# Performance work log

Measured on AMD Instinct MI355X. Metric: run time of the kernel, lower is better.

The kernel has to match this reference:

```python
import jax, jax.numpy as jnp
import numpy as np

B, T, M, P = 256, 256, 256, 256  # batch, timesteps, encoder hidden m, decoder hidden p


def setup_inputs() -> dict:
    key = jax.random.key(0)
    ks = jax.random.split(key, 12)
    def n(k, shape, s=0.05):
        return jax.random.normal(k, shape, dtype=jnp.float32) * s
    return {
        "data": n(ks[0], (B, T - 1, 1), 1.0),          # decoder inputs y_1..y_{T-1}
        "encoder_h": n(ks[1], (B, T, M), 1.0),          # encoder hidden states
        "h0": jnp.zeros((B, P), jnp.float32),
        "s0": jnp.zeros((B, P), jnp.float32),
        # dense: Dense(1) on concat([x, context]) -> input dim 1+M
        "Wd": n(ks[2], (1 + M, 1)), "bd": jnp.zeros((1,), jnp.float32),
        # decoder LSTM (Keras gate order i,f,c,o): kernel (1,4P), recurrent (P,4P)
        "Wk": n(ks[3], (1, 4 * P)), "Wr": n(ks[4], (P, 4 * P)), "bl": jnp.zeros((4 * P,), jnp.float32),
        # temporal attention: W: 2P->M, U: M->M, v: M->1
        "Ww": n(ks[5], (2 * P, M)), "bw": jnp.zeros((M,), jnp.float32),
        "Wu": n(ks[6], (M, M)), "bu": jnp.zeros((M,), jnp.float32),
        "Wv": n(ks[7], (M, 1)), "bv": jnp.zeros((1,), jnp.float32),
        # output head: densevb: P+M -> 1, denseWb: 1 -> P
        "Wvb": n(ks[8], (P + M, 1)), "bvb": jnp.zeros((1,), jnp.float32),
        "Wwb": n(ks[9], (1, P)), "bwb": jnp.zeros((P,), jnp.float32),
    }


def reference(data, encoder_h, h0, s0, Wd, bd, Wk, Wr, bl, Ww, bw,
              Wu, bu, Wv, bv, Wvb, bvb, Wwb, bwb):
    # Hoist U(encoder_h) out of the time loop: it does not depend on t (same math).
    Ue = encoder_h @ Wu + bu                      # (B, T, M)
    xs = jnp.transpose(data, (1, 0, 2))           # (T-1, B, 1) for scan
    ctx0 = jnp.zeros((data.shape[0], Ue.shape[-1]), data.dtype)  # initial context (B, M)

    def step(carry, x_t):
        h, s, ctx = carry                          # (B,P), (B,P), (B,M)
        # y_tilde = Dense(1)(concat([x_t, context]))
        y = jnp.concatenate([x_t, ctx], axis=-1) @ Wd + bd        # (B, 1)
        # single-step Keras LSTM cell, gates i, f, c, o
        z = y @ Wk + h @ Wr + bl                   # (B, 4P)
        i, f, g, o = jnp.split(z, 4, axis=-1)
        s_new = jax.nn.sigmoid(f) * s + jax.nn.sigmoid(i) * jnp.tanh(g)
        h_new = jax.nn.sigmoid(o) * jnp.tanh(s_new)
        # temporal attention: l = v(tanh(W(repeat(concat[h,s])) + U(encoder_h)))
        dsc = jnp.concatenate([h_new, s_new], axis=-1) @ Ww + bw  # (B, M)
        l = jnp.tanh(dsc[:, None, :] + Ue) @ Wv + bv              # (B, T, 1)
        beta = jax.nn.softmax(l, axis=1)                          # softmax over time axis
        # context = beta^T @ encoder_h -> (B, M)
        ctx_new = jnp.sum(beta * encoder_h, axis=1)
        return (h_new, s_new, ctx_new), None

    (h, s, ctx), _ = jax.lax.scan(step, (h0, s0, ctx0), xs)
    cat = jnp.concatenate([h, ctx], axis=-1)[:, None, :]          # (B, 1, P+M)
    # denseWb(densevb(concatenated)): (P+M)->1 then 1->P, as in the source
    return (cat @ Wvb + bvb) @ Wwb + bwb                          # (B, 1, P)
```

## Files before the change

### kernel.cpp

```cpp
#include <hip/hip_runtime.h>
#include <hip/hip_bf16.h>

#define B 256
#define T 256
#define M 256
#define P 256
#define TSTEPS 255
#define NT 1024

typedef unsigned int uint;
typedef _Float16 hf2 __attribute__((ext_vector_type(2)));

__device__ __forceinline__ float fast_tanh(float x) {
    float e = exp2f(x * 2.885390082f);
    return 1.f - 2.f * __builtin_amdgcn_rcpf(e + 1.f);
}
__device__ __forceinline__ float fast_sigmoid(float x) {
    float e = exp2f(-x * 1.442695041f);
    return __builtin_amdgcn_rcpf(1.f + e);
}

#if defined(__has_builtin)
#if __has_builtin(__builtin_amdgcn_fdot2)
#define HAVE_FDOT2 1
#endif
#endif

__device__ __forceinline__ float dot2(uint a, uint b, float c) {
#ifdef HAVE_FDOT2
    return __builtin_amdgcn_fdot2(__builtin_bit_cast(hf2, a),
                                  __builtin_bit_cast(hf2, b), c, false);
#else
    hf2 x = __builtin_bit_cast(hf2, a), y = __builtin_bit_cast(hf2, b);
    return c + (float)x.x * (float)y.x + (float)x.y * (float)y.y;
#endif
}

__device__ __forceinline__ uint pk16(float a, float b) {
    return __builtin_bit_cast(uint, __builtin_amdgcn_cvt_pkrtz(a, b));
}

__global__ __launch_bounds__(256) void ue_gemm(
    const float* __restrict__ enc, const float* __restrict__ Wu,
    const float* __restrict__ bu, _Float16* __restrict__ Ue16)
{
    __shared__ float At[32][256];
    const int r0 = blockIdx.x * 32;
    const int tid = threadIdx.x;

    #pragma unroll 4
    for (int i = 0; i < 32; ++i)
        At[i][tid] = enc[(size_t)(r0 + i) * 256 + tid];
    __syncthreads();

    float acc[32];
    #pragma unroll
    for (int r = 0; r < 32; ++r) acc[r] = 0.f;

    for (int k = 0; k < 256; k += 4) {
        float w0 = Wu[(size_t)(k + 0) * 256 + tid];
        float w1 = Wu[(size_t)(k + 1) * 256 + tid];
        float w2 = Wu[(size_t)(k + 2) * 256 + tid];
        float w3 = Wu[(size_t)(k + 3) * 256 + tid];
        #pragma unroll
        for (int r = 0; r < 32; ++r) {
            float4 a4 = *(const float4*)&At[r][k];
            acc[r] += a4.x * w0 + a4.y * w1 + a4.z * w2 + a4.w * w3;
        }
    }
    float bub = bu[tid];
    #pragma unroll 4
    for (int r = 0; r < 32; ++r)
        Ue16[(size_t)(r0 + r) * 256 + tid] =
            (_Float16)exp2f(1.442695041f * (acc[r] + bub));
}

__global__ __launch_bounds__(256) void wr_cvt(
    const float* __restrict__ Wr, uint4* __restrict__ Wsz)
{
    int i = blockIdx.x * 256 + threadIdx.x;
    int kc = i >> 10, c = i & 1023;
    const float* s = Wr + (size_t)kc * 8 * 1024 + c;
    uint4 o;
    o.x = pk16(s[0 * 1024], s[1 * 1024]);
    o.y = pk16(s[2 * 1024], s[3 * 1024]);
    o.z = pk16(s[4 * 1024], s[5 * 1024]);
    o.w = pk16(s[6 * 1024], s[7 * 1024]);
    Wsz[i] = o;
}

__global__ __launch_bounds__(256) void ww_cvt(
    const float* __restrict__ Ww, uint4* __restrict__ Wwsz)
{
    int i = blockIdx.x * 256 + threadIdx.x;
    int kk = i >> 8, m = i & 255;
    const float* s = Ww + (size_t)kk * 8 * 256 + m;
    uint4 o;
    o.x = pk16(s[0 * 256], s[1 * 256]);
    o.y = pk16(s[2 * 256], s[3 * 256]);
    o.z = pk16(s[4 * 256], s[5 * 256]);
    o.w = pk16(s[6 * 256], s[7 * 256]);
    Wwsz[i] = o;
}

__global__ __launch_bounds__(NT, 4) void decoder_scan(
    const float* __restrict__ data,
    const float* __restrict__ h0,  const float* __restrict__ s0,
    const float* __restrict__ Wd,  const float* __restrict__ bd,
    const float* __restrict__ Wk,  const float* __restrict__ bl,
    const float* __restrict__ bw,
    const float* __restrict__ Wv,  const float* __restrict__ bv,
    const float* __restrict__ Wvb, const float* __restrict__ bvb,
    const float* __restrict__ Wwb, const float* __restrict__ bwb,
    const float* __restrict__ enc,
    const _Float16* __restrict__ Ue16g,
    const uint4* __restrict__ Wsz, const uint4* __restrict__ Wwsz,
    float* __restrict__ out)
{
    const int b    = blockIdx.x;
    const int tid  = threadIdx.x;
    const int lane = tid & 63;
    const int wave = tid >> 6;

    __shared__ _Float16 ue_lds[T * M];
    __shared__ float h_lds[P], s_lds[P];
    __shared__ __align__(16) uint hs2[128 + 4 + 128];
    __shared__ float z_lds[4 * 257];
    __shared__ __align__(16) uint  edup[2][132];
    __shared__ __align__(16) float wv2dup[2][264];
    __shared__ float el_lds[T];
    __shared__ float g_lds[T];
    __shared__ float ctx_lds[M];
    __shared__ __align__(16) float sred[8], yred[8];
    __shared__ float ya[4];
    __shared__ float data_lds[TSTEPS + 1];

    uint* h2_lds = hs2;
    uint* s2_lds = hs2 + 132;

    {
        const uint4* src = (const uint4*)(Ue16g + (size_t)b * T * M);
        uint4* dst = (uint4*)ue_lds;
        #pragma unroll
        for (int i = 0; i < 8; ++i) {
            int g = tid + i * NT;
            uint4 v = src[g];
            int r = g >> 5, lin = g & 31;
            int phys = (lin & 16) | ((lin ^ (2 * r + (lin >> 4))) & 15);
            dst[(r << 5) + phys] = v;
        }
    }
    if (tid < 256) {
        float hv = h0[b * 256 + tid], sv = s0[b * 256 + tid];
        h_lds[tid] = hv; s_lds[tid] = sv; ctx_lds[tid] = 0.f;
        float w2 = 2.f * Wv[tid];
        wv2dup[0][tid] = w2; wv2dup[1][tid] = w2;
        float hv1 = __shfl_down(hv, 1, 64);
        float sv1 = __shfl_down(sv, 1, 64);
        if (!(tid & 1)) {
            h2_lds[tid >> 1] = pk16(hv, hv1);
            s2_lds[tid >> 1] = pk16(sv, sv1);
        }
    }
    if (tid < 8) { sred[tid] = 1.f; yred[tid] = 0.f; }
    if (tid < TSTEPS) data_lds[tid] = data[b * TSTEPS + tid];

    const float Wd0 = Wd[0], bd0 = bd[0];
    const int   gate = tid & 3, uu = tid >> 2;
    const int   cp  = gate * 256 + uu;
    const int   cpi = gate * 257 + uu;
    const float wkp = Wk[cp], blp = bl[cp];

    const float* encB = enc + (size_t)b * T * M;

    {
        float w0 = Wd[1 + lane * 4], w1 = Wd[2 + lane * 4];
        float w2 = Wd[3 + lane * 4], w3 = Wd[4 + lane * 4];
        for (int i = 0; i < 16; ++i) {
            int tp = wave * 16 + i;
            float4 e4 = *(const float4*)&encB[(size_t)tp * 256 + lane * 4];
            float p = e4.x * w0 + e4.y * w1 + e4.z * w2 + e4.w * w3;
            #pragma unroll
            for (int mm = 32; mm >= 1; mm >>= 1) p += __shfl_xor(p, mm, 64);
            if (lane == 0) g_lds[tp] = p;
        }
    }
    __syncthreads();

    const uint4* h2u4 = (const uint4*)h2_lds;
    const uint4* s2u4 = (const uint4*)s2_lds;

    {
        const uint4* wc = Wsz + tid;
        float acc = 0.f;
        #pragma unroll 4
        for (int kc = 0; kc < 32; ++kc) {
            uint4 w = wc[kc << 10];
            uint4 h = h2u4[kc];
            acc = dot2(w.x, h.x, acc); acc = dot2(w.y, h.y, acc);
            acc = dot2(w.z, h.z, acc); acc = dot2(w.w, h.w, acc);
        }
        z_lds[(tid >> 8) * 257 + (tid & 255)] = acc;
    }
    __syncthreads();

    const int aw  = wave - 8;
    const int aid = (tid >= 512) ? (tid - 512) : 0;
    const int dm  = aid >> 1;
    const int dkh = aid & 1;
    const int ekey = aid & 15;
    const float bwm = bw[dm];
    const uint4* wwp  = Wwsz + (dkh << 13) + dm;
    const uint4* uecT = (const uint4*)ue_lds + (aid << 4);
    const uint4*  edT = (const uint4*)(&edup[dkh][0]) + (dkh << 4);
    const float4* wvT = (const float4*)(&wv2dup[dkh][0]) + (dkh << 5);
    const uint4* wcA = Wsz + tid;
    const uint4* wcB = Wsz + tid + 512;

    float accA = 0.f, accB = 0.f;

    for (int t = 0; t < TSTEPS; ++t) {
        {
            float4 sa = *(const float4*)&sred[0], sb = *(const float4*)&sred[4];
            float4 yaa = *(const float4*)&yred[0], yab = *(const float4*)&yred[4];
            float S = sa.x + sa.y + sa.z + sa.w + sb.x + sb.y + sb.z + sb.w;
            float Y = yaa.x + yaa.y + yaa.z + yaa.w + yab.x + yab.y + yab.z + yab.w;
            float ys = Y * __builtin_amdgcn_rcpf(S) + data_lds[t] * Wd0 + bd0;
            float zc = z_lds[cpi] + ys * wkp + blp;
            float nl = (gate == 2) ? fast_tanh(zc) : fast_sigmoid(zc);
            float n1 = __shfl_xor(nl, 1, 64);
            float n2 = __shfl_xor(nl, 2, 64);
            float n3 = __shfl_xor(nl, 3, 64);
            float hn = 0.f, snv = 0.f;
            if (gate == 0) {
                float s_old = s_lds[uu];
                snv = n1 * s_old + nl * n2;
                hn  = n3 * fast_tanh(snv);
                s_lds[uu] = snv; h_lds[uu] = hn;
            }
            float hn4 = __shfl_down(hn, 4, 64);
            float sn4 = __shfl_down(snv, 4, 64);
            if ((tid & 7) == 0) {
                h2_lds[uu >> 1] = pk16(hn, hn4);
                s2_lds[uu >> 1] = pk16(snv, sn4);
            }
        }
        __syncthreads();

        if (wave < 8) {
            accA = 0.f; accB = 0.f;
            #pragma unroll 4
            for (int kc = 0; kc < 16; ++kc) {
                uint4 wA = wcA[kc << 10], wB = wcB[kc << 10];
                uint4 h = h2u4[kc];
                accA = dot2(wA.x, h.x, accA); accA = dot2(wA.y, h.y, accA);
                accA = dot2(wA.z, h.z, accA); accA = dot2(wA.w, h.w, accA);
                accB = dot2(wB.x, h.x, accB); accB = dot2(wB.y, h.y, accB);
                accB = dot2(wB.z, h.z, accB); accB = dot2(wB.w, h.w, accB);
            }
        } else {
            const uint4* cat4 = dkh ? s2u4 : h2u4;
            float a = 0.f;
            #pragma unroll 8
            for (int i = 0; i < 32; ++i) {
                uint4 w = wwp[i << 8];
                uint4 c = cat4[i];
                a = dot2(w.x, c.x, a); a = dot2(w.y, c.y, a);
                a = dot2(w.z, c.z, a); a = dot2(w.w, c.w, a);
            }
            a += __shfl_xor(a, 1, 64);
            float ed = exp2f(1.442695041f * (a + bwm));
            float ed2 = __shfl_xor(ed, 2, 64);
            if ((aid & 3) == 0) {
                uint u = pk16(ed, ed2);
                edup[0][dm >> 1] = u;
                edup[1][dm >> 1] = u;
            }
        }
        __syncthreads();

        if (wave < 8) {
            #pragma unroll 4
            for (int kc = 16; kc < 32; ++kc) {
                uint4 wA = wcA[kc << 10], wB = wcB[kc << 10];
                uint4 h = h2u4[kc];
                accA = dot2(wA.x, h.x, accA); accA = dot2(wA.y, h.y, accA);
                accA = dot2(wA.z, h.z, accA); accA = dot2(wA.w, h.w, accA);
                accB = dot2(wB.x, h.x, accB); accB = dot2(wB.y, h.y, accB);
                accB = dot2(wB.z, h.z, accB); accB = dot2(wB.w, h.w, accB);
            }
            z_lds[(tid >> 8) * 257 + (tid & 255)] = accA;
            z_lds[(2 + (tid >> 8)) * 257 + (tid & 255)] = accB;
        } else {
            __builtin_amdgcn_s_setprio(1);
            float pl = 0.f;
            #pragma unroll 4
            for (int jj = 0; jj < 16; ++jj) {
                uint4 u = uecT[jj ^ ekey];
                uint4 d = edT[jj];
                float4 wA = wvT[jj * 2], wB = wvT[jj * 2 + 1];
                hf2 p0 = __builtin_bit_cast(hf2, u.x) * __builtin_bit_cast(hf2, d.x);
                hf2 p1 = __builtin_bit_cast(hf2, u.y) * __builtin_bit_cast(hf2, d.y);
                hf2 p2 = __builtin_bit_cast(hf2, u.z) * __builtin_bit_cast(hf2, d.z);
                hf2 p3 = __builtin_bit_cast(hf2, u.w) * __builtin_bit_cast(hf2, d.w);
                p0 = p0 * p0; p1 = p1 * p1; p2 = p2 * p2; p3 = p3 * p3;
                {
                    float a0 = fminf((float)p0.x, 1e18f) + 1.f;
                    float a1 = fminf((float)p0.y, 1e18f) + 1.f;
                    float qq = __builtin_amdgcn_rcpf(a0 * a1);
                    pl = fmaf(wA.x, a1 * qq, pl);
                    pl = fmaf(wA.y, a0 * qq, pl);
                }
                {
                    float a0 = fminf((float)p1.x, 1e18f) + 1.f;
                    float a1 = fminf((float)p1.y, 1e18f) + 1.f;
                    float qq = __builtin_amdgcn_rcpf(a0 * a1);
                    pl = fmaf(wA.z, a1 * qq, pl);
                    pl = fmaf(wA.w, a0 * qq, pl);
                }
                {
                    float a0 = fminf((float)p2.x, 1e18f) + 1.f;
                    float a1 = fminf((float)p2.y, 1e18f) + 1.f;
                    float qq = __builtin_amdgcn_rcpf(a0 * a1);
                    pl = fmaf(wB.x, a1 * qq, pl);
                    pl = fmaf(wB.y, a0 * qq, pl);
                }
                {
                    float a0 = fminf((float)p3.x, 1e18f) + 1.f;
                    float a1 = fminf((float)p3.y, 1e18f) + 1.f;
                    float qq = __builtin_amdgcn_rcpf(a0 * a1);
                    pl = fmaf(wB.z, a1 * qq, pl);
                    pl = fmaf(wB.w, a0 * qq, pl);
                }
            }
            pl += __shfl_xor(pl, 1, 64);
            float ev = exp2f(-1.442695041f * pl);
            if (!dkh) el_lds[dm] = ev;
            float yg = ev * g_lds[dm];
            #pragma unroll
            for (int mm = 2; mm <= 32; mm <<= 1) {
                ev += __shfl_xor(ev, mm, 64);
                yg += __shfl_xor(yg, mm, 64);
            }
            if (lane == 0) { sred[aw] = ev; yred[aw] = yg; }
            __builtin_amdgcn_s_setprio(0);
        }
        __syncthreads();
    }

    {
        float S;
        {
            float4 sa = *(const float4*)&sred[0], sb = *(const float4*)&sred[4];
            S = sa.x + sa.y + sa.z + sa.w + sb.x + sb.y + sb.z + sb.w;
        }
        float a0 = 0.f, a1 = 0.f, a2 = 0.f, a3 = 0.f;
        for (int i = 0; i < 16; ++i) {
            int tp = wave * 16 + i;
            float w = el_lds[tp];
            float4 e4 = *(const float4*)&encB[(size_t)tp * 256 + lane * 4];
            a0 += w * e4.x; a1 += w * e4.y; a2 += w * e4.z; a3 += w * e4.w;
        }
        atomicAdd(&ctx_lds[lane * 4 + 0], a0);
        atomicAdd(&ctx_lds[lane * 4 + 1], a1);
        atomicAdd(&ctx_lds[lane * 4 + 2], a2);
        atomicAdd(&ctx_lds[lane * 4 + 3], a3);
        __syncthreads();

        float qp = 0.f;
        if (tid < 256) {
            float ctx = ctx_lds[tid] * __builtin_amdgcn_rcpf(S);
            qp = h_lds[tid] * Wvb[tid] + ctx * Wvb[256 + tid];
        }
        if (wave < 4) {
            #pragma unroll
            for (int mm = 32; mm >= 1; mm >>= 1) qp += __shfl_xor(qp, mm, 64);
            if (lane == 0) ya[wave] = qp;
        }
        __syncthreads();
        if (tid < 256) {
            float qv = ya[0] + ya[1] + ya[2] + ya[3] + bvb[0];
            out[b * 256 + tid] = qv * Wwb[tid] + bwb[tid];
        }
    }
}

extern "C" void kernel_launch(void* const* d_in, const int* in_sizes, int n_in,
                              void* d_out, int out_size, void* d_ws, size_t ws_size,
                              hipStream_t stream) {
    const float* data = (const float*)d_in[0];
    const float* enc  = (const float*)d_in[1];
    const float* h0   = (const float*)d_in[2];
    const float* s0   = (const float*)d_in[3];
    const float* Wd   = (const float*)d_in[4];
    const float* bd   = (const float*)d_in[5];
    const float* Wk   = (const float*)d_in[6];
    const float* Wr   = (const float*)d_in[7];
    const float* bl   = (const float*)d_in[8];
    const float* Ww   = (const float*)d_in[9];
    const float* bw   = (const float*)d_in[10];
    const float* Wu   = (const float*)d_in[11];
    const float* bu   = (const float*)d_in[12];
    const float* Wv   = (const float*)d_in[13];
    const float* bv   = (const float*)d_in[14];
    const float* Wvb  = (const float*)d_in[15];
    const float* bvb  = (const float*)d_in[16];
    const float* Wwb  = (const float*)d_in[17];
    const float* bwb  = (const float*)d_in[18];

    _Float16* Ue16 = (_Float16*)d_ws;
    uint4* Wsz  = (uint4*)((char*)d_ws + (32ull << 20));
    uint4* Wwsz = (uint4*)((char*)d_ws + (32ull << 20) + (512ull << 10));
    float* out = (float*)d_out;

    hipLaunchKernelGGL(ue_gemm, dim3((B * T) / 32), dim3(256), 0, stream,
                       enc, Wu, bu, Ue16);
    hipLaunchKernelGGL(wr_cvt, dim3(128), dim3(256), 0, stream, Wr, Wsz);
    hipLaunchKernelGGL(ww_cvt, dim3(64), dim3(256), 0, stream, Ww, Wwsz);
    hipLaunchKernelGGL(decoder_scan, dim3(B), dim3(NT), 0, stream,
                       data, h0, s0, Wd, bd, Wk, bl, bw,
                       Wv, bv, Wvb, bvb, Wwb, bwb,
                       enc, Ue16, Wsz, Wwsz, out);
}
```

Measured before the change: 2.848 ms.

## Split recurrence and attention waves with spin-flag sync and register-cached weights

```diff
diff --git a/kernel.cpp b/kernel.cpp
--- a/kernel.cpp
+++ b/kernel.cpp
@@ -7,6 +7,8 @@
 #define P 256
 #define TSTEPS 255
 #define NT 1024
+#define RG 6
+#define RA 8
 
 typedef unsigned int uint;
 typedef _Float16 hf2 __attribute__((ext_vector_type(2)));
@@ -134,6 +136,7 @@
     __shared__ __align__(16) float sred[8], yred[8];
     __shared__ float ya[4];
     __shared__ float data_lds[TSTEPS + 1];
+    __shared__ int aflag;
 
     uint* h2_lds = hs2;
     uint* s2_lds = hs2 + 132;
@@ -150,6 +153,7 @@
             dst[(r << 5) + phys] = v;
         }
     }
+    if (tid == 0) aflag = 0;
     if (tid < 256) {
         float hv = h0[b * 256 + tid], sv = s0[b * 256 + tid];
         h_lds[tid] = hv; s_lds[tid] = sv; ctx_lds[tid] = 0.f;
@@ -166,11 +170,6 @@
     if (tid < TSTEPS) data_lds[tid] = data[b * TSTEPS + tid];
 
     const float Wd0 = Wd[0], bd0 = bd[0];
-    const int   gate = tid & 3, uu = tid >> 2;
-    const int   cp  = gate * 256 + uu;
-    const int   cpi = gate * 257 + uu;
-    const float wkp = Wk[cp], blp = bl[cp];
-
     const float* encB = enc + (size_t)b * T * M;
 
     {
@@ -204,65 +203,134 @@
     }
     __syncthreads();
 
-    const int aw  = wave - 8;
-    const int aid = (tid >= 512) ? (tid - 512) : 0;
-    const int dm  = aid >> 1;
-    const int dkh = aid & 1;
-    const int ekey = aid & 15;
-    const float bwm = bw[dm];
-    const uint4* wwp  = Wwsz + (dkh << 13) + dm;
-    const uint4* uecT = (const uint4*)ue_lds + (aid << 4);
-    const uint4*  edT = (const uint4*)(&edup[dkh][0]) + (dkh << 4);
-    const float4* wvT = (const float4*)(&wv2dup[dkh][0]) + (dkh << 5);
-    const uint4* wcA = Wsz + tid;
-    const uint4* wcB = Wsz + tid + 512;
-
-    float accA = 0.f, accB = 0.f;
-
-    for (int t = 0; t < TSTEPS; ++t) {
-        {
-            float4 sa = *(const float4*)&sred[0], sb = *(const float4*)&sred[4];
-            float4 yaa = *(const float4*)&yred[0], yab = *(const float4*)&yred[4];
-            float S = sa.x + sa.y + sa.z + sa.w + sb.x + sb.y + sb.z + sb.w;
-            float Y = yaa.x + yaa.y + yaa.z + yaa.w + yab.x + yab.y + yab.z + yab.w;
-            float ys = Y * __builtin_amdgcn_rcpf(S) + data_lds[t] * Wd0 + bd0;
-            float zc = z_lds[cpi] + ys * wkp + blp;
-            float nl = (gate == 2) ? fast_tanh(zc) : fast_sigmoid(zc);
-            float n1 = __shfl_xor(nl, 1, 64);
-            float n2 = __shfl_xor(nl, 2, 64);
-            float n3 = __shfl_xor(nl, 3, 64);
-            float hn = 0.f, snv = 0.f;
-            if (gate == 0) {
-                float s_old = s_lds[uu];
-                snv = n1 * s_old + nl * n2;
-                hn  = n3 * fast_tanh(snv);
-                s_lds[uu] = snv; h_lds[uu] = hn;
-            }
-            float hn4 = __shfl_down(hn, 4, 64);
-            float sn4 = __shfl_down(snv, 4, 64);
-            if ((tid & 7) == 0) {
-                h2_lds[uu >> 1] = pk16(hn, hn4);
-                s2_lds[uu >> 1] = pk16(snv, sn4);
-            }
-        }
-        __syncthreads();
-
-        if (wave < 8) {
-            accA = 0.f; accB = 0.f;
+    if (wave < 8) {
+        const int gate = tid & 3, uu0 = tid >> 2, uu1 = uu0 + 128;
+        const int cz0 = gate * 257 + uu0, cz1 = gate * 257 + uu1;
+        const float wk0 = Wk[gate * 256 + uu0], bl0 = bl[gate * 256 + uu0];
+        const float wk1 = Wk[gate * 256 + uu1], bl1 = bl[gate * 256 + uu1];
+        const int zr = tid >> 8, zc = tid & 255;
+        const uint4* wcA = Wsz + tid;
+        const uint4* wcB = Wsz + tid + 512;
+        uint4 rA[RG], rB[RG];
+        #pragma unroll
+        for (int kc = 0; kc < RG; ++kc) { rA[kc] = wcA[kc << 10]; rB[kc] = wcB[kc << 10]; }
+
+        for (int t = 0; t < TSTEPS; ++t) {
+            uint4 pA0 = wcA[(RG + 0) << 10], pB0 = wcB[(RG + 0) << 10];
+            uint4 pA1 = wcA[(RG + 1) << 10], pB1 = wcB[(RG + 1) << 10];
+
+            {
+                float4 sa = *(const float4*)&sred[0], sb = *(const float4*)&sred[4];
+                float4 yaa = *(const float4*)&yred[0], yab = *(const float4*)&yred[4];
+                float S = sa.x + sa.y + sa.z + sa.w + sb.x + sb.y + sb.z + sb.w;
+                float Y = yaa.x + yaa.y + yaa.z + yaa.w + yab.x + yab.y + yab.z + yab.w;
+                float ys = Y * __builtin_amdgcn_rcpf(S) + data_lds[t] * Wd0 + bd0;
+                float zc0 = z_lds[cz0] + ys * wk0 + bl0;
+                float zc1 = z_lds[cz1] + ys * wk1 + bl1;
+                float nl0 = (gate == 2) ? fast_tanh(zc0) : fast_sigmoid(zc0);
+                float nl1 = (gate == 2) ? fast_tanh(zc1) : fast_sigmoid(zc1);
+                float a1 = __shfl_xor(nl0, 1, 64);
+                float a2 = __shfl_xor(nl0, 2, 64);
+                float a3 = __shfl_xor(nl0, 3, 64);
+                float b1 = __shfl_xor(nl1, 1, 64);
+                float b2 = __shfl_xor(nl1, 2, 64);
+                float b3 = __shfl_xor(nl1, 3, 64);
+                float hn0 = 0.f, sv0 = 0.f, hn1 = 0.f, sv1 = 0.f;
+                if (gate == 0) {
+                    sv0 = a1 * s_lds[uu0] + nl0 * a2;
+                    hn0 = a3 * fast_tanh(sv0);
+                    sv1 = b1 * s_lds[uu1] + nl1 * b2;
+                    hn1 = b3 * fast_tanh(sv1);
+                    s_lds[uu0] = sv0; h_lds[uu0] = hn0;
+                    s_lds[uu1] = sv1; h_lds[uu1] = hn1;
+                }
+                float hd0 = __shfl_down(hn0, 4, 64), sd0 = __shfl_down(sv0, 4, 64);
+                float hd1 = __shfl_down(hn1, 4, 64), sd1 = __shfl_down(sv1, 4, 64);
+                if ((tid & 7) == 0) {
+                    h2_lds[uu0 >> 1] = pk16(hn0, hd0); s2_lds[uu0 >> 1] = pk16(sv0, sd0);
+                    h2_lds[uu1 >> 1] = pk16(hn1, hd1); s2_lds[uu1 >> 1] = pk16(sv1, sd1);
+                }
+            }
+            __syncthreads();
+            float a0 = 0.f, a1 = 0.f;
+            #pragma unroll
+            for (int kc = 0; kc < RG; ++kc) {
+                uint4 h = h2u4[kc];
+                a0 = dot2(rA[kc].x, h.x, a0); a0 = dot2(rA[kc].y, h.y, a0);
+                a0 = dot2(rA[kc].z, h.z, a0); a0 = dot2(rA[kc].w, h.w, a0);
+                a1 = dot2(rB[kc].x, h.x, a1); a1 = dot2(rB[kc].y, h.y, a1);
+                a1 = dot2(rB[kc].z, h.z, a1); a1 = dot2(rB[kc].w, h.w, a1);
+            }
+            {
+                uint4 h = h2u4[RG];
+                a0 = dot2(pA0.x, h.x, a0); a0 = dot2(pA0.y, h.y, a0);
+                a0 = dot2(pA0.z, h.z, a0); a0 = dot2(pA0.w, h.w, a0);
+                a1 = dot2(pB0.x, h.x, a1); a1 = dot2(pB0.y, h.y, a1);
+                a1 = dot2(pB0.z, h.z, a1); a1 = dot2(pB0.w, h.w, a1);
+            }
+            {
+                uint4 h = h2u4[RG + 1];
+                a0 = dot2(pA1.x, h.x, a0); a0 = dot2(pA1.y, h.y, a0);
+                a0 = dot2(pA1.z, h.z, a0); a0 = dot2(pA1.w, h.w, a0);
+                a1 = dot2(pB1.x, h.x, a1); a1 = dot2(pB1.y, h.y, a1);
+                a1 = dot2(pB1.z, h.z, a1); a1 = dot2(pB1.w, h.w, a1);
+            }
             #pragma unroll 4
-            for (int kc = 0; kc < 16; ++kc) {
+            for (int kc = RG + 2; kc < 32; ++kc) {
                 uint4 wA = wcA[kc << 10], wB = wcB[kc << 10];
                 uint4 h = h2u4[kc];
-                accA = dot2(wA.x, h.x, accA); accA = dot2(wA.y, h.y, accA);
-                accA = dot2(wA.z, h.z, accA); accA = dot2(wA.w, h.w, accA);
-                accB = dot2(wB.x, h.x, accB); accB = dot2(wB.y, h.y, accB);
-                accB = dot2(wB.z, h.z, accB); accB = dot2(wB.w, h.w, accB);
-            }
-        } else {
-            const uint4* cat4 = dkh ? s2u4 : h2u4;
+                a0 = dot2(wA.x, h.x, a0); a0 = dot2(wA.y, h.y, a0);
+                a0 = dot2(wA.z, h.z, a0); a0 = dot2(wA.w, h.w, a0);
+                a1 = dot2(wB.x, h.x, a1); a1 = dot2(wB.y, h.y, a1);
+                a1 = dot2(wB.z, h.z, a1); a1 = dot2(wB.w, h.w, a1);
+            }
+            z_lds[zr * 257 + zc] = a0;
+            z_lds[(2 + zr) * 257 + zc] = a1;
+            __syncthreads();
+        }
+    } else {
+        const int aw  = wave - 8;
+        const int aid = tid - 512;
+        const int dm  = aid >> 1;
+        const int dkh = aid & 1;
+        const int ekey = aid & 15;
+        const float bwm = bw[dm];
+        const uint4* wwp  = Wwsz + (dkh << 13) + dm;
+        const uint4* uecT = (const uint4*)ue_lds + (aid << 4);
+        const uint4*  edT = (const uint4*)(&edup[dkh][0]) + (dkh << 4);
+        const float4* wvT = (const float4*)(&wv2dup[dkh][0]) + (dkh << 5);
+        const uint4* cat4 = dkh ? s2u4 : h2u4;
+        uint4 rW[RA];
+        #pragma unroll
+        for (int i = 0; i < RA; ++i) rW[i] = wwp[i << 8];
+
+        for (int t = 0; t < TSTEPS; ++t) {
+            uint4 e0 = wwp[(RA + 0) << 8], e1 = wwp[(RA + 1) << 8];
+            uint4 e2 = wwp[(RA + 2) << 8], e3 = wwp[(RA + 3) << 8];
+            __syncthreads();
             float a = 0.f;
-            #pragma unroll 8
-            for (int i = 0; i < 32; ++i) {
+            #pragma unroll
+            for (int i = 0; i < RA; ++i) {
+                uint4 c = cat4[i];
+                a = dot2(rW[i].x, c.x, a); a = dot2(rW[i].y, c.y, a);
+                a = dot2(rW[i].z, c.z, a); a = dot2(rW[i].w, c.w, a);
+            }
+            {
+                uint4 c = cat4[RA + 0];
+                a = dot2(e0.x, c.x, a); a = dot2(e0.y, c.y, a);
+                a = dot2(e0.z, c.z, a); a = dot2(e0.w, c.w, a);
+                c = cat4[RA + 1];
+                a = dot2(e1.x, c.x, a); a = dot2(e1.y, c.y, a);
+                a = dot2(e1.z, c.z, a); a = dot2(e1.w, c.w, a);
+                c = cat4[RA + 2];
+                a = dot2(e2.x, c.x, a); a = dot2(e2.y, c.y, a);
+                a = dot2(e2.z, c.z, a); a = dot2(e2.w, c.w, a);
+                c = cat4[RA + 3];
+                a = dot2(e3.x, c.x, a); a = dot2(e3.y, c.y, a);
+                a = dot2(e3.z, c.z, a); a = dot2(e3.w, c.w, a);
+            }
+            #pragma unroll 4
+            for (int i = RA + 4; i < 32; ++i) {
                 uint4 w = wwp[i << 8];
                 uint4 c = cat4[i];
                 a = dot2(w.x, c.x, a); a = dot2(w.y, c.y, a);
@@ -276,22 +344,12 @@
                 edup[0][dm >> 1] = u;
                 edup[1][dm >> 1] = u;
             }
-        }
-        __syncthreads();
-
-        if (wave < 8) {
-            #pragma unroll 4
-            for (int kc = 16; kc < 32; ++kc) {
-                uint4 wA = wcA[kc << 10], wB = wcB[kc << 10];
-                uint4 h = h2u4[kc];
-                accA = dot2(wA.x, h.x, accA); accA = dot2(wA.y, h.y, accA);
-                accA = dot2(wA.z, h.z, accA); accA = dot2(wA.w, h.w, accA);
-                accB = dot2(wB.x, h.x, accB); accB = dot2(wB.y, h.y, accB);
-                accB = dot2(wB.z, h.z, accB); accB = dot2(wB.w, h.w, accB);
-            }
-            z_lds[(tid >> 8) * 257 + (tid & 255)] = accA;
-            z_lds[(2 + (tid >> 8)) * 257 + (tid & 255)] = accB;
-        } else {
+            __threadfence_block();
+            if (lane == 0) atomicAdd(&aflag, 1);
+            const int tgt = 8 * (t + 1);
+            while (*(volatile int*)&aflag < tgt) {}
+            __threadfence_block();
+
             __builtin_amdgcn_s_setprio(1);
             float pl = 0.f;
             #pragma unroll 4
@@ -344,8 +402,8 @@
             }
             if (lane == 0) { sred[aw] = ev; yred[aw] = yg; }
             __builtin_amdgcn_s_setprio(0);
-        }
-        __syncthreads();
+            __syncthreads();
+        }
     }
 
     {
```

New measurement: 2.820 ms. Within noise of the previous version (-1.0%).
